# Kernel tuning notes

Hardware: AMD Instinct MI355X
Metric: run time of the kernel (lower is better)

## Reference

```python
import jax, jax.numpy as jnp
import numpy as np

N = 50000   # nodes
E = 800000  # edges (before self-loops)
IN_C, HID, OUT_C = 10, 96, 48


def setup_inputs() -> dict:
    key = jax.random.key(0)
    ks = jax.random.split(key, 8)
    x = jax.random.normal(ks[0], (N, IN_C), dtype=jnp.float32)
    edge_index = jax.random.randint(ks[1], (2, E), 0, N, dtype=jnp.int64)
    # Glorot-ish scaled weights for the three GCN layers
    W1 = jax.random.normal(ks[2], (IN_C, HID), dtype=jnp.float32) * (1.0 / np.sqrt(IN_C))
    b1 = jnp.zeros((HID,), dtype=jnp.float32)
    W_mu = jax.random.normal(ks[3], (HID, OUT_C), dtype=jnp.float32) * (1.0 / np.sqrt(HID))
    b_mu = jnp.zeros((OUT_C,), dtype=jnp.float32)
    W_logstd = jax.random.normal(ks[4], (HID, OUT_C), dtype=jnp.float32) * (1.0 / np.sqrt(HID))
    b_logstd = jnp.zeros((OUT_C,), dtype=jnp.float32)
    return {"x": x, "edge_index": edge_index, "W1": W1, "b1": b1,
            "W_mu": W_mu, "b_mu": b_mu, "W_logstd": W_logstd, "b_logstd": b_logstd}


def _gcn_norm(edge_index, n_nodes, dtype):
    # PyG gcn_norm: add self-loops, symmetric normalization D^-1/2 A D^-1/2
    loops = jnp.arange(n_nodes, dtype=edge_index.dtype)
    ei = jnp.concatenate([edge_index, jnp.stack([loops, loops])], axis=1)
    row, col = ei[0], ei[1]
    deg = jax.ops.segment_sum(jnp.ones(ei.shape[1], dtype=dtype), col, num_segments=n_nodes)
    dis = jnp.where(deg > 0, jax.lax.rsqrt(deg), jnp.zeros_like(deg))
    norm = dis[row] * dis[col]  # [E+N]
    return row, col, norm


def _gcn_conv(h, row, col, norm, W, b, n_nodes):
    hw = h @ W                                   # dense projection [N, F_out]
    msgs = hw[row] * norm[:, None]               # gather + scale   [E+N, F_out]
    out = jax.ops.segment_sum(msgs, col, num_segments=n_nodes)  # scatter-add
    return out + b


def reference(x, edge_index, W1, b1, W_mu, b_mu, W_logstd, b_logstd):
    row, col, norm = _gcn_norm(edge_index, N, x.dtype)
    h = jax.nn.relu(_gcn_conv(x, row, col, norm, W1, b1, N))
    mu = _gcn_conv(h, row, col, norm, W_mu, b_mu, N)
    logstd = _gcn_conv(h, row, col, norm, W_logstd, b_logstd, N)
    return mu, logstd
```

## Files before the change

kernel.cpp:

```cpp
#include <hip/hip_runtime.h>
#include <hip/hip_bf16.h>

#define NND 50000
#define NED 800000
#define INC 10
#define HID 96
#define OUTC 48
#define NOUT (NND*OUTC)
#define MTILES 3125
#define NW 98
#define SPAN 512
#define EW_CAP 9216
#define PB 200
#define PBE 4000

typedef __hip_bfloat16 bf16;
typedef __attribute__((ext_vector_type(8))) short short8;
typedef __attribute__((ext_vector_type(4))) float f32x4;

#define W1F_O  0L
#define B1F_O  960L
#define BMF_O  1056L
#define BLF_O  1104L
#define DIS_O  1152L
#define XS_O   51152L
#define FLOATS_TOT 551152L

__device__ __forceinline__ float b2f(bf16 v) { return __bfloat162float(v); }
__device__ __forceinline__ float bfLo(unsigned int p) { return __uint_as_float(p << 16); }
__device__ __forceinline__ float bfHi(unsigned int p) { return __uint_as_float(p & 0xffff0000u); }
__device__ __forceinline__ unsigned short f2bu(float v) {
    return __bfloat16_as_ushort(__float2bfloat16(v));
}

__global__ __launch_bounds__(1024) void k_part(const int* ei, const void* x,
                                               const void* w1, const void* b1,
                                               const void* wm, const void* bm,
                                               const void* wl, const void* bl,
                                               int* flags, float* F, unsigned short* wct,
                                               unsigned int* part, int* smat, int* cmat) {
    __shared__ int s_oddnz, s_big;
    __shared__ int counts[NW], cur[NW];
    __shared__ unsigned int buf[PBE];
    int tid = threadIdx.x;
    if (tid == 0) { s_oddnz = 0; s_big = 0; }
    if (tid < NW) counts[tid] = 0;
    __syncthreads();
    {
        if (tid < 128) {
            if (ei[2 * tid + 1] != 0) atomicOr(&s_oddnz, 1);
        }
        if (tid < 256) {
            const unsigned short* xs = (const unsigned short*)x;
            unsigned short u = xs[tid * 8];
            float f = __uint_as_float(((unsigned int)u) << 16);
            int big = !(fabsf(f) < 64.0f);
            unsigned short u2 = xs[tid * 8 + 5];
            float f2 = __uint_as_float(((unsigned int)u2) << 16);
            big |= !(fabsf(f2) < 64.0f);
            if (big) atomicOr(&s_big, 1);
        }
    }
    __syncthreads();
    int iw = (s_oddnz == 0) ? 1 : 0;
    int ff = s_big ? 1 : 0;
    if (blockIdx.x == 0 && tid == 0) { flags[0] = iw; flags[1] = ff; }

    if (blockIdx.x < 11) {
        int idx = blockIdx.x * 1024 + tid;
        if (idx < 10368) {
            const void* src; long off; int mode; long dst = 0;
            if      (idx < 960)  { src = w1; off = idx;        mode = 0; dst = W1F_O + idx; }
            else if (idx < 1056) { src = b1; off = idx - 960;  mode = 0; dst = B1F_O + (idx - 960); }
            else if (idx < 1104) { src = bm; off = idx - 1056; mode = 0; dst = BMF_O + (idx - 1056); }
            else if (idx < 1152) { src = bl; off = idx - 1104; mode = 0; dst = BLF_O + (idx - 1104); }
            else if (idx < 5760) { src = wm; off = idx - 1152; mode = 1; }
            else                 { src = wl; off = idx - 5760; mode = 2; }
            float v = ff ? ((const float*)src)[off] : b2f(((const bf16*)src)[off]);
            if (mode == 0) F[dst] = v;
            else if (mode == 1) wct[(off % OUTC) * (long)HID + off / OUTC] = f2bu(v);
            else                wct[(OUTC + off % OUTC) * (long)HID + off / OUTC] = f2bu(v);
        }
    }

    unsigned int wreg[4];
    int base = blockIdx.x * 1000;
    int j = tid;
    if (j < 1000) {
        int j4 = base + j;
        int r0, r1, r2, r3, c0, c1, c2, c3;
        if (iw) {
            const int4* pr = (const int4*)ei;
            const int4* pc = (const int4*)(ei + 2L * NED);
            int4 ra = pr[2 * j4], rb = pr[2 * j4 + 1];
            int4 ca = pc[2 * j4], cb = pc[2 * j4 + 1];
            r0 = ra.x; r1 = ra.z; r2 = rb.x; r3 = rb.z;
            c0 = ca.x; c1 = ca.z; c2 = cb.x; c3 = cb.z;
        } else {
            int4 ra = ((const int4*)ei)[j4];
            int4 ca = ((const int4*)(ei + NED))[j4];
            r0 = ra.x; r1 = ra.y; r2 = ra.z; r3 = ra.w;
            c0 = ca.x; c1 = ca.y; c2 = ca.z; c3 = ca.w;
        }
        wreg[0] = (unsigned)r0 | ((unsigned)c0 << 16);
        wreg[1] = (unsigned)r1 | ((unsigned)c1 << 16);
        wreg[2] = (unsigned)r2 | ((unsigned)c2 << 16);
        wreg[3] = (unsigned)r3 | ((unsigned)c3 << 16);
        atomicAdd(&counts[wreg[0] >> 25], 1);
        atomicAdd(&counts[wreg[1] >> 25], 1);
        atomicAdd(&counts[wreg[2] >> 25], 1);
        atomicAdd(&counts[wreg[3] >> 25], 1);
    }
    __syncthreads();
    if (tid < NW) {
        int run = 0;
        for (int jj = 0; jj < tid; ++jj) run += counts[jj];
        cur[tid] = run;
        cmat[tid * PB + blockIdx.x] = counts[tid];
        smat[tid * PB + blockIdx.x] = blockIdx.x * PBE + run;
    }
    __syncthreads();
    if (j < 1000) {
#pragma unroll
        for (int q = 0; q < 4; ++q) {
            unsigned int w = wreg[q];
            int pos = atomicAdd(&cur[w >> 25], 1);
            buf[pos] = w;
        }
    }
    __syncthreads();
    for (int i = tid; i < PBE; i += 1024) part[blockIdx.x * PBE + i] = buf[i];
}

__global__ __launch_bounds__(1024) void k_win(const unsigned int* part, const int* smat,
                                              const int* cmat, const void* x, float* F,
                                              int* cnt, int* start, unsigned short* csr) {
    __shared__ int Lrun[PB], Srun[PB];
    __shared__ int hist[SPAN], cur[SPAN];
    __shared__ float dl[SPAN];
    __shared__ int wsum[8];
    __shared__ int s_big;
    int tid = threadIdx.x;
    int w = blockIdx.x;
    if (tid == 0) s_big = 0;
    if (tid < PB) { Lrun[tid] = cmat[w * PB + tid]; Srun[tid] = smat[w * PB + tid]; }
    if (tid < SPAN) hist[tid] = 0;
    __syncthreads();
    if (tid < 256) {
        const unsigned short* xs = (const unsigned short*)x;
        unsigned short u = xs[tid * 8];
        float f = __uint_as_float(((unsigned int)u) << 16);
        int big = !(fabsf(f) < 64.0f);
        unsigned short u2 = xs[tid * 8 + 5];
        float f2 = __uint_as_float(((unsigned int)u2) << 16);
        big |= !(fabsf(f2) < 64.0f);
        if (big) atomicOr(&s_big, 1);
    }
    unsigned int lo = (unsigned)w * SPAN;
    int wave = tid >> 6, lane = tid & 63;
    for (int rb = wave; rb < PB; rb += 16) {
        int L = Lrun[rb], S = Srun[rb];
        for (int i = lane; i < L; i += 64)
            atomicAdd(&hist[(part[S + i] >> 16) - lo], 1);
    }
    __syncthreads();
    int ff = s_big;
    int v = 0;
    if (tid < SPAN) {
        v = hist[tid];
#pragma unroll
        for (int d = 1; d < 64; d <<= 1) {
            int t = __shfl_up(v, d, 64);
            if (lane >= d) v += t;
        }
        if (lane == 63) wsum[wave] = v;
    }
    __syncthreads();
    if (tid < 8) {
        int sv = wsum[tid];
#pragma unroll
        for (int d = 1; d < 8; d <<= 1) {
            int t = __shfl_up(sv, d, 64);
            if (tid >= d) sv += t;
        }
        wsum[tid] = sv;
    }
    __syncthreads();
    if (tid < SPAN) {
        int stv = v + (wave ? wsum[wave - 1] : 0);
        int h0 = hist[tid];
        int abs0 = w * EW_CAP + (stv - h0);
        cur[tid] = abs0;
        float dis = rsqrtf((float)h0 + 1.0f);
        dl[tid] = dis;
        int g = (int)lo + tid;
        if (g < NND) {
            cnt[g] = h0; start[g] = abs0;
            F[DIS_O + g] = dis;
        }
    }
    __syncthreads();
    for (int i = tid; i < SPAN * INC; i += 1024) {
        int node = (int)lo + i / INC;
        if (node < NND) {
            long xo = (long)node * INC + (i % INC);
            float xv = ff ? ((const float*)x)[xo] : b2f(((const bf16*)x)[xo]);
            F[XS_O + xo] = dl[i / INC] * xv;
        }
    }
    int lim = (w + 1) * EW_CAP;
    for (int rb = wave; rb < PB; rb += 16) {
        int L = Lrun[rb], S = Srun[rb];
        for (int i = lane; i < L; i += 64) {
            unsigned int e = part[S + i];
            int pos = atomicAdd(&cur[(e >> 16) - lo], 1);
            if (pos < lim) csr[pos] = (unsigned short)(e & 0xffffu);
        }
    }
}

__global__ __launch_bounds__(256) void k_layer1(const int* cnt, const int* start,
                                                const unsigned short* csr, const float* F,
                                                unsigned short* h) {
    __shared__ float w1s[1056];
    for (int i = threadIdx.x; i < 1056; i += 256) w1s[i] = F[W1F_O + i];
    __syncthreads();
    int idx = blockIdx.x * 256 + threadIdx.x;
    if (idx >= NND * 4) return;
    int node = idx >> 2, sub = idx & 3;
    int s = start[node], t = s + cnt[node];
    int lim = ((node >> 9) + 1) * EW_CAP;
    if (t > lim) t = lim;
    float ax[INC];
#pragma unroll
    for (int j = 0; j < INC; ++j) ax[j] = 0.0f;
    for (int k = s + sub; k < t; k += 4) {
        int src = csr[k];
        const float2* xr = (const float2*)(F + XS_O + (long)src * INC);
#pragma unroll
        for (int j = 0; j < 5; ++j) {
            float2 v = xr[j];
            ax[2 * j]     += v.x;
            ax[2 * j + 1] += v.y;
        }
    }
    if (sub == 0) {
        const float2* xr = (const float2*)(F + XS_O + (long)node * INC);
#pragma unroll
        for (int j = 0; j < 5; ++j) {
            float2 v = xr[j];
            ax[2 * j]     += v.x;
            ax[2 * j + 1] += v.y;
        }
    }
#pragma unroll
    for (int j = 0; j < INC; ++j) {
        ax[j] += __shfl_xor(ax[j], 1, 64);
        ax[j] += __shfl_xor(ax[j], 2, 64);
    }
    float dn = F[DIS_O + node];
#pragma unroll
    for (int j = 0; j < INC; ++j) ax[j] *= dn;
    int f0 = sub * 24;
    unsigned int* hrow = (unsigned int*)(h + (size_t)node * HID);
#pragma unroll
    for (int f = f0; f < f0 + 24; f += 2) {
        float a0 = w1s[960 + f], a1 = w1s[960 + f + 1];
#pragma unroll
        for (int kk = 0; kk < INC; ++kk) {
            a0 = fmaf(ax[kk], w1s[kk * HID + f], a0);
            a1 = fmaf(ax[kk], w1s[kk * HID + f + 1], a1);
        }
        a0 = fmaxf(a0, 0.0f) * dn;
        a1 = fmaxf(a1, 0.0f) * dn;
        unsigned int u0 = f2bu(a0), u1 = f2bu(a1);
        hrow[f >> 1] = u0 | (u1 << 16);
    }
}

__global__ __launch_bounds__(256) void k_gh(const int* cnt, const int* start,
                                            const unsigned short* csr, const float* F,
                                            const unsigned short* h, const unsigned short* wct,
                                            const int* flags, void* dout) {
    int wid = threadIdx.x >> 6;
    int lane = threadIdx.x & 63;
    int mtile = blockIdx.x * 4 + wid;
    if (mtile >= MTILES) return;
    int l16 = lane & 15, quad = lane >> 4;
    int node = mtile * 16 + l16;

    const uint4* hb4 = (const uint4*)h;
    long rowq = (long)node * 12;

    int s = start[node], c = cnt[node];
    int lim = ((node >> 9) + 1) * EW_CAP;
    if (s + c > lim) c = lim - s;

    float acc[3][8];
    {
        uint4 p0 = hb4[rowq + quad];
        uint4 p1 = hb4[rowq + 4 + quad];
        uint4 p2 = hb4[rowq + 8 + quad];
#pragma unroll
        for (int t = 0; t < 4; ++t) {
            unsigned int w0 = (t == 0) ? p0.x : (t == 1) ? p0.y : (t == 2) ? p0.z : p0.w;
            unsigned int w1 = (t == 0) ? p1.x : (t == 1) ? p1.y : (t == 2) ? p1.z : p1.w;
            unsigned int w2 = (t == 0) ? p2.x : (t == 1) ? p2.y : (t == 2) ? p2.z : p2.w;
            acc[0][2 * t] = bfLo(w0); acc[0][2 * t + 1] = bfHi(w0);
            acc[1][2 * t] = bfLo(w1); acc[1][2 * t + 1] = bfHi(w1);
            acc[2][2 * t] = bfLo(w2); acc[2][2 * t + 1] = bfHi(w2);
        }
    }
    int k = 0;
    for (; k + 1 < c; k += 2) {
        int s0 = csr[s + k], s1 = csr[s + k + 1];
        long r0 = (long)s0 * 12, r1 = (long)s1 * 12;
        uint4 a0 = hb4[r0 + quad], a1 = hb4[r0 + 4 + quad], a2 = hb4[r0 + 8 + quad];
        uint4 b0 = hb4[r1 + quad], b1 = hb4[r1 + 4 + quad], b2 = hb4[r1 + 8 + quad];
#pragma unroll
        for (int t = 0; t < 4; ++t) {
            unsigned int w0 = (t == 0) ? a0.x : (t == 1) ? a0.y : (t == 2) ? a0.z : a0.w;
            unsigned int w1 = (t == 0) ? a1.x : (t == 1) ? a1.y : (t == 2) ? a1.z : a1.w;
            unsigned int w2 = (t == 0) ? a2.x : (t == 1) ? a2.y : (t == 2) ? a2.z : a2.w;
            acc[0][2 * t] += bfLo(w0); acc[0][2 * t + 1] += bfHi(w0);
            acc[1][2 * t] += bfLo(w1); acc[1][2 * t + 1] += bfHi(w1);
            acc[2][2 * t] += bfLo(w2); acc[2][2 * t + 1] += bfHi(w2);
        }
#pragma unroll
        for (int t = 0; t < 4; ++t) {
            unsigned int w0 = (t == 0) ? b0.x : (t == 1) ? b0.y : (t == 2) ? b0.z : b0.w;
            unsigned int w1 = (t == 0) ? b1.x : (t == 1) ? b1.y : (t == 2) ? b1.z : b1.w;
            unsigned int w2 = (t == 0) ? b2.x : (t == 1) ? b2.y : (t == 2) ? b2.z : b2.w;
            acc[0][2 * t] += bfLo(w0); acc[0][2 * t + 1] += bfHi(w0);
            acc[1][2 * t] += bfLo(w1); acc[1][2 * t + 1] += bfHi(w1);
            acc[2][2 * t] += bfLo(w2); acc[2][2 * t + 1] += bfHi(w2);
        }
    }
    if (k < c) {
        int s0 = csr[s + k];
        long r0 = (long)s0 * 12;
        uint4 a0 = hb4[r0 + quad], a1 = hb4[r0 + 4 + quad], a2 = hb4[r0 + 8 + quad];
#pragma unroll
        for (int t = 0; t < 4; ++t) {
            unsigned int w0 = (t == 0) ? a0.x : (t == 1) ? a0.y : (t == 2) ? a0.z : a0.w;
            unsigned int w1 = (t == 0) ? a1.x : (t == 1) ? a1.y : (t == 2) ? a1.z : a1.w;
            unsigned int w2 = (t == 0) ? a2.x : (t == 1) ? a2.y : (t == 2) ? a2.z : a2.w;
            acc[0][2 * t] += bfLo(w0); acc[0][2 * t + 1] += bfHi(w0);
            acc[1][2 * t] += bfLo(w1); acc[1][2 * t + 1] += bfHi(w1);
            acc[2][2 * t] += bfLo(w2); acc[2][2 * t + 1] += bfHi(w2);
        }
    }
    float dn = F[DIS_O + node];
    short8 af[3];
#pragma unroll
    for (int g = 0; g < 3; ++g)
#pragma unroll
        for (int j = 0; j < 8; ++j)
            af[g][j] = (short)f2bu(acc[g][j] * dn);

    int ff = flags[1];
#pragma unroll
    for (int nt = 0; nt < 6; ++nt) {
        const unsigned short* wb = wct + ((size_t)nt * 16 + l16) * HID + quad * 8;
        short8 b0 = *(const short8*)(wb);
        short8 b1 = *(const short8*)(wb + 32);
        short8 b2 = *(const short8*)(wb + 64);
        f32x4 cacc = {0.0f, 0.0f, 0.0f, 0.0f};
        cacc = __builtin_amdgcn_mfma_f32_16x16x32_bf16(af[0], b0, cacc, 0, 0, 0);
        cacc = __builtin_amdgcn_mfma_f32_16x16x32_bf16(af[1], b1, cacc, 0, 0, 0);
        cacc = __builtin_amdgcn_mfma_f32_16x16x32_bf16(af[2], b2, cacc, 0, 0, 0);
        int n = nt * 16 + l16;
        float bias = (n < OUTC) ? F[BMF_O + n] : F[BLF_O + n - OUTC];
        long obase = (n < OUTC) ? ((long)n) : (NOUT + (long)(n - OUTC));
#pragma unroll
        for (int r = 0; r < 4; ++r) {
            int m = mtile * 16 + quad * 4 + r;
            float val = cacc[r] + bias;
            long oi = (long)m * OUTC + obase;
            if (ff) ((float*)dout)[oi] = val;
            else    ((bf16*)dout)[oi] = __float2bfloat16(val);
        }
    }
}

extern "C" void kernel_launch(void* const* d_in, const int* in_sizes, int n_in,
                              void* d_out, int out_size, void* d_ws, size_t ws_size,
                              hipStream_t stream) {
    const int* ei = (const int*)d_in[1];
    int* flags = (int*)d_ws;
    float* F = (float*)((char*)d_ws + 256);
    unsigned short* h   = (unsigned short*)(F + FLOATS_TOT);
    unsigned short* wct = h + (size_t)NND * HID;
    int* cnt   = (int*)(wct + (size_t)HID * HID);
    int* start = cnt + NND;
    unsigned int* part = (unsigned int*)(start + NND);
    int* smat = (int*)(part + NED);
    int* cmat = smat + NW * PB;
    unsigned short* csr = (unsigned short*)(cmat + NW * PB);

    k_part<<<PB, 1024, 0, stream>>>(ei, d_in[0], d_in[2], d_in[3], d_in[4],
                                    d_in[5], d_in[6], d_in[7], flags, F, wct,
                                    part, smat, cmat);
    k_win<<<NW, 1024, 0, stream>>>(part, smat, cmat, d_in[0], F, cnt, start, csr);
    k_layer1<<<(NND * 4 + 255) / 256, 256, 0, stream>>>(cnt, start, csr, F, h);
    k_gh<<<(MTILES + 3) / 4, 256, 0, stream>>>(cnt, start, csr, F, h, wct, flags, d_out);
}
```

Baseline: 148.9 us.

## Split neighbor gathers across more threads and two waves per tile

Layer-1 aggregation now uses 8 threads per node instead of 4, with two gathers issued per loop step and an extra shuffle stage. The gather-matmul kernel assigns two waves per 16-node tile, each taking alternating edges with a 4-way unrolled load loop, and merges partial sums through shared memory before the MFMA step. The aim is more memory-level parallelism and shorter per-wave edge chains to hide gather latency, at the cost of an extra block sync, shared-memory traffic, and idle second waves during the MFMA phase.

```diff
diff --git a/kernel.cpp b/kernel.cpp
--- a/kernel.cpp
+++ b/kernel.cpp
@@ -32,6 +32,22 @@
 __device__ __forceinline__ unsigned short f2bu(float v) {
     return __bfloat16_as_ushort(__float2bfloat16(v));
 }
+
+#define ACCADD(Q0, Q1, Q2) do {                                             \
+    const uint4 q0 = (Q0), q1 = (Q1), q2 = (Q2);                            \
+    acc[0][0] += bfLo(q0.x); acc[0][1] += bfHi(q0.x);                       \
+    acc[0][2] += bfLo(q0.y); acc[0][3] += bfHi(q0.y);                       \
+    acc[0][4] += bfLo(q0.z); acc[0][5] += bfHi(q0.z);                       \
+    acc[0][6] += bfLo(q0.w); acc[0][7] += bfHi(q0.w);                       \
+    acc[1][0] += bfLo(q1.x); acc[1][1] += bfHi(q1.x);                       \
+    acc[1][2] += bfLo(q1.y); acc[1][3] += bfHi(q1.y);                       \
+    acc[1][4] += bfLo(q1.z); acc[1][5] += bfHi(q1.z);                       \
+    acc[1][6] += bfLo(q1.w); acc[1][7] += bfHi(q1.w);                       \
+    acc[2][0] += bfLo(q2.x); acc[2][1] += bfHi(q2.x);                       \
+    acc[2][2] += bfLo(q2.y); acc[2][3] += bfHi(q2.y);                       \
+    acc[2][4] += bfLo(q2.z); acc[2][5] += bfHi(q2.z);                       \
+    acc[2][6] += bfLo(q2.w); acc[2][7] += bfHi(q2.w);                       \
+} while (0)
 
 __global__ __launch_bounds__(1024) void k_part(const int* ei, const void* x,
                                                const void* w1, const void* b1,
@@ -226,17 +242,39 @@
     for (int i = threadIdx.x; i < 1056; i += 256) w1s[i] = F[W1F_O + i];
     __syncthreads();
     int idx = blockIdx.x * 256 + threadIdx.x;
-    if (idx >= NND * 4) return;
-    int node = idx >> 2, sub = idx & 3;
+    if (idx >= NND * 8) return;
+    int node = idx >> 3, sub = idx & 7;
     int s = start[node], t = s + cnt[node];
     int lim = ((node >> 9) + 1) * EW_CAP;
     if (t > lim) t = lim;
     float ax[INC];
 #pragma unroll
     for (int j = 0; j < INC; ++j) ax[j] = 0.0f;
-    for (int k = s + sub; k < t; k += 4) {
-        int src = csr[k];
-        const float2* xr = (const float2*)(F + XS_O + (long)src * INC);
+    int k = s + sub;
+    for (; k + 8 < t; k += 16) {
+        int s0 = csr[k], s1 = csr[k + 8];
+        const float2* x0 = (const float2*)(F + XS_O + (long)s0 * INC);
+        const float2* x1 = (const float2*)(F + XS_O + (long)s1 * INC);
+        float2 a0 = x0[0], a1 = x0[1], a2 = x0[2], a3 = x0[3], a4 = x0[4];
+        float2 b0 = x1[0], b1 = x1[1], b2 = x1[2], b3 = x1[3], b4 = x1[4];
+        ax[0] += a0.x + b0.x; ax[1] += a0.y + b0.y;
+        ax[2] += a1.x + b1.x; ax[3] += a1.y + b1.y;
+        ax[4] += a2.x + b2.x; ax[5] += a2.y + b2.y;
+        ax[6] += a3.x + b3.x; ax[7] += a3.y + b3.y;
+        ax[8] += a4.x + b4.x; ax[9] += a4.y + b4.y;
+    }
+    if (k < t) {
+        int s0 = csr[k];
+        const float2* x0 = (const float2*)(F + XS_O + (long)s0 * INC);
+#pragma unroll
+        for (int j = 0; j < 5; ++j) {
+            float2 v = x0[j];
+            ax[2 * j]     += v.x;
+            ax[2 * j + 1] += v.y;
+        }
+    }
+    if (sub == 0) {
+        const float2* xr = (const float2*)(F + XS_O + (long)node * INC);
 #pragma unroll
         for (int j = 0; j < 5; ++j) {
             float2 v = xr[j];
@@ -244,27 +282,19 @@
             ax[2 * j + 1] += v.y;
         }
     }
-    if (sub == 0) {
-        const float2* xr = (const float2*)(F + XS_O + (long)node * INC);
-#pragma unroll
-        for (int j = 0; j < 5; ++j) {
-            float2 v = xr[j];
-            ax[2 * j]     += v.x;
-            ax[2 * j + 1] += v.y;
-        }
-    }
 #pragma unroll
     for (int j = 0; j < INC; ++j) {
         ax[j] += __shfl_xor(ax[j], 1, 64);
         ax[j] += __shfl_xor(ax[j], 2, 64);
+        ax[j] += __shfl_xor(ax[j], 4, 64);
     }
     float dn = F[DIS_O + node];
 #pragma unroll
     for (int j = 0; j < INC; ++j) ax[j] *= dn;
-    int f0 = sub * 24;
+    int f0 = sub * 12;
     unsigned int* hrow = (unsigned int*)(h + (size_t)node * HID);
 #pragma unroll
-    for (int f = f0; f < f0 + 24; f += 2) {
+    for (int f = f0; f < f0 + 12; f += 2) {
         float a0 = w1s[960 + f], a1 = w1s[960 + f + 1];
 #pragma unroll
         for (int kk = 0; kk < INC; ++kk) {
@@ -278,14 +308,14 @@
     }
 }
 
-__global__ __launch_bounds__(256) void k_gh(const int* cnt, const int* start,
+__global__ __launch_bounds__(128) void k_gh(const int* cnt, const int* start,
                                             const unsigned short* csr, const float* F,
                                             const unsigned short* h, const unsigned short* wct,
                                             const int* flags, void* dout) {
-    int wid = threadIdx.x >> 6;
+    __shared__ float4 red[64][6];
+    int half = threadIdx.x >> 6;
     int lane = threadIdx.x & 63;
-    int mtile = blockIdx.x * 4 + wid;
-    if (mtile >= MTILES) return;
+    int mtile = blockIdx.x;
     int l16 = lane & 15, quad = lane >> 4;
     int node = mtile * 16 + l16;
 
@@ -297,58 +327,45 @@
     if (s + c > lim) c = lim - s;
 
     float acc[3][8];
-    {
-        uint4 p0 = hb4[rowq + quad];
-        uint4 p1 = hb4[rowq + 4 + quad];
-        uint4 p2 = hb4[rowq + 8 + quad];
-#pragma unroll
-        for (int t = 0; t < 4; ++t) {
-            unsigned int w0 = (t == 0) ? p0.x : (t == 1) ? p0.y : (t == 2) ? p0.z : p0.w;
-            unsigned int w1 = (t == 0) ? p1.x : (t == 1) ? p1.y : (t == 2) ? p1.z : p1.w;
-            unsigned int w2 = (t == 0) ? p2.x : (t == 1) ? p2.y : (t == 2) ? p2.z : p2.w;
-            acc[0][2 * t] = bfLo(w0); acc[0][2 * t + 1] = bfHi(w0);
-            acc[1][2 * t] = bfLo(w1); acc[1][2 * t + 1] = bfHi(w1);
-            acc[2][2 * t] = bfLo(w2); acc[2][2 * t + 1] = bfHi(w2);
-        }
-    }
-    int k = 0;
-    for (; k + 1 < c; k += 2) {
-        int s0 = csr[s + k], s1 = csr[s + k + 1];
-        long r0 = (long)s0 * 12, r1 = (long)s1 * 12;
-        uint4 a0 = hb4[r0 + quad], a1 = hb4[r0 + 4 + quad], a2 = hb4[r0 + 8 + quad];
-        uint4 b0 = hb4[r1 + quad], b1 = hb4[r1 + 4 + quad], b2 = hb4[r1 + 8 + quad];
-#pragma unroll
-        for (int t = 0; t < 4; ++t) {
-            unsigned int w0 = (t == 0) ? a0.x : (t == 1) ? a0.y : (t == 2) ? a0.z : a0.w;
-            unsigned int w1 = (t == 0) ? a1.x : (t == 1) ? a1.y : (t == 2) ? a1.z : a1.w;
-            unsigned int w2 = (t == 0) ? a2.x : (t == 1) ? a2.y : (t == 2) ? a2.z : a2.w;
-            acc[0][2 * t] += bfLo(w0); acc[0][2 * t + 1] += bfHi(w0);
-            acc[1][2 * t] += bfLo(w1); acc[1][2 * t + 1] += bfHi(w1);
-            acc[2][2 * t] += bfLo(w2); acc[2][2 * t + 1] += bfHi(w2);
-        }
-#pragma unroll
-        for (int t = 0; t < 4; ++t) {
-            unsigned int w0 = (t == 0) ? b0.x : (t == 1) ? b0.y : (t == 2) ? b0.z : b0.w;
-            unsigned int w1 = (t == 0) ? b1.x : (t == 1) ? b1.y : (t == 2) ? b1.z : b1.w;
-            unsigned int w2 = (t == 0) ? b2.x : (t == 1) ? b2.y : (t == 2) ? b2.z : b2.w;
-            acc[0][2 * t] += bfLo(w0); acc[0][2 * t + 1] += bfHi(w0);
-            acc[1][2 * t] += bfLo(w1); acc[1][2 * t + 1] += bfHi(w1);
-            acc[2][2 * t] += bfLo(w2); acc[2][2 * t + 1] += bfHi(w2);
-        }
-    }
-    if (k < c) {
-        int s0 = csr[s + k];
-        long r0 = (long)s0 * 12;
-        uint4 a0 = hb4[r0 + quad], a1 = hb4[r0 + 4 + quad], a2 = hb4[r0 + 8 + quad];
-#pragma unroll
-        for (int t = 0; t < 4; ++t) {
-            unsigned int w0 = (t == 0) ? a0.x : (t == 1) ? a0.y : (t == 2) ? a0.z : a0.w;
-            unsigned int w1 = (t == 0) ? a1.x : (t == 1) ? a1.y : (t == 2) ? a1.z : a1.w;
-            unsigned int w2 = (t == 0) ? a2.x : (t == 1) ? a2.y : (t == 2) ? a2.z : a2.w;
-            acc[0][2 * t] += bfLo(w0); acc[0][2 * t + 1] += bfHi(w0);
-            acc[1][2 * t] += bfLo(w1); acc[1][2 * t + 1] += bfHi(w1);
-            acc[2][2 * t] += bfLo(w2); acc[2][2 * t + 1] += bfHi(w2);
-        }
+#pragma unroll
+    for (int g = 0; g < 3; ++g)
+#pragma unroll
+        for (int j = 0; j < 8; ++j) acc[g][j] = 0.0f;
+    if (half == 0) {
+        ACCADD(hb4[rowq + quad], hb4[rowq + 4 + quad], hb4[rowq + 8 + quad]);
+    }
+    int k = half;
+    for (; k + 6 < c; k += 8) {
+        int e0 = csr[s + k], e1 = csr[s + k + 2], e2 = csr[s + k + 4], e3 = csr[s + k + 6];
+        long r0 = (long)e0 * 12, r1 = (long)e1 * 12, r2 = (long)e2 * 12, r3 = (long)e3 * 12;
+        uint4 x00 = hb4[r0 + quad], x01 = hb4[r0 + 4 + quad], x02 = hb4[r0 + 8 + quad];
+        uint4 x10 = hb4[r1 + quad], x11 = hb4[r1 + 4 + quad], x12 = hb4[r1 + 8 + quad];
+        uint4 x20 = hb4[r2 + quad], x21 = hb4[r2 + 4 + quad], x22 = hb4[r2 + 8 + quad];
+        uint4 x30 = hb4[r3 + quad], x31 = hb4[r3 + 4 + quad], x32 = hb4[r3 + 8 + quad];
+        ACCADD(x00, x01, x02);
+        ACCADD(x10, x11, x12);
+        ACCADD(x20, x21, x22);
+        ACCADD(x30, x31, x32);
+    }
+    for (; k < c; k += 2) {
+        int e0 = csr[s + k];
+        long r0 = (long)e0 * 12;
+        ACCADD(hb4[r0 + quad], hb4[r0 + 4 + quad], hb4[r0 + 8 + quad]);
+    }
+    if (half == 1) {
+#pragma unroll
+        for (int g = 0; g < 3; ++g) {
+            red[lane][2 * g]     = make_float4(acc[g][0], acc[g][1], acc[g][2], acc[g][3]);
+            red[lane][2 * g + 1] = make_float4(acc[g][4], acc[g][5], acc[g][6], acc[g][7]);
+        }
+    }
+    __syncthreads();
+    if (half == 1) return;
+#pragma unroll
+    for (int g = 0; g < 3; ++g) {
+        float4 u = red[lane][2 * g], v = red[lane][2 * g + 1];
+        acc[g][0] += u.x; acc[g][1] += u.y; acc[g][2] += u.z; acc[g][3] += u.w;
+        acc[g][4] += v.x; acc[g][5] += v.y; acc[g][6] += v.z; acc[g][7] += v.w;
     }
     float dn = F[DIS_O + node];
     short8 af[3];
@@ -402,6 +419,6 @@
                                     d_in[5], d_in[6], d_in[7], flags, F, wct,
                                     part, smat, cmat);
     k_win<<<NW, 1024, 0, stream>>>(part, smat, cmat, d_in[0], F, cnt, start, csr);
-    k_layer1<<<(NND * 4 + 255) / 256, 256, 0, stream>>>(cnt, start, csr, F, h);
-    k_gh<<<(MTILES + 3) / 4, 256, 0, stream>>>(cnt, start, csr, F, h, wct, flags, d_out);
-}
+    k_layer1<<<(NND * 8 + 255) / 256, 256, 0, stream>>>(cnt, start, csr, F, h);
+    k_gh<<<MTILES, 128, 0, stream>>>(cnt, start, csr, F, h, wct, flags, d_out);
+}
```

Measured after the change: 145.0 us. 1.03x faster.
